# Performance work log

Hardware: AMD Instinct MI355X
Metric: run time of the kernel (lower is better)

Reference implementation:

```python
import jax, jax.numpy as jnp
import numpy as np
import math

B, T, E = 2, 2048, 2048
G, QPG, D = 4, 4, 128  # kv groups, queries per group, head dim (G*QPG*D == E)


def sinusoidal_pe(t, d, dtype):
    pos = jnp.arange(t, dtype=jnp.float32)[:, None]            # [T,1]
    i = jnp.arange(0, d, 2, dtype=jnp.float32)                 # [D/2]
    inv_freq = jnp.exp(-(jnp.log(10000.0) * i / d))            # [D/2]
    ang = pos * inv_freq                                       # [T,D/2]
    pe = jnp.zeros((t, d), dtype=jnp.float32)
    pe = pe.at[:, 0::2].set(jnp.sin(ang)).at[:, 1::2].set(jnp.cos(ang))
    return pe.astype(dtype)


def setup_inputs() -> dict:
    key = jax.random.key(0)
    ks = jax.random.split(key, 6)
    s = lambda fan_in: 1.0 / math.sqrt(fan_in)
    return {
        "x":   jax.random.normal(ks[0], (B, T, E), dtype=jnp.float32),
        "wq":  jax.random.uniform(ks[1], (E, G * QPG * D), jnp.float32, -s(E), s(E)),
        "bq":  jax.random.uniform(ks[2], (G * QPG * D,), jnp.float32, -s(E), s(E)),
        "wkv": jax.random.uniform(ks[3], (E, 2 * G * D), jnp.float32, -s(E), s(E)),
        "bkv": jax.random.uniform(ks[4], (2 * G * D,), jnp.float32, -s(E), s(E)),
        "wo":  jax.random.uniform(ks[5], (G * QPG * D, E), jnp.float32, -s(G * QPG * D), s(G * QPG * D)),
    }


def reference(x, wq, bq, wkv, bkv, wo):
    b, t, e = x.shape
    # projections
    q = (x @ wq + bq).reshape(b, t, G, QPG, D).transpose(0, 2, 3, 1, 4)   # [B,G,QPG,T,D]
    kv = (x @ wkv + bkv).reshape(b, t, G, 1, 2 * D).transpose(0, 2, 3, 1, 4)  # [B,G,1,T,2D]
    k, v = kv[..., :D], kv[..., D:]                                       # [B,G,1,T,D]
    # inline additive sinusoidal positional embedding on q and k
    pe = sinusoidal_pe(t, D, x.dtype)                                     # [T,D]
    q = q + pe
    k = k + pe
    # scores: [B,G,QPG,T,T] (kv head axis k has size 1, summed out)
    scores = jnp.einsum('bgqtd,bgksd->bgqts', q, k) / math.sqrt(D)
    causal = jnp.tril(jnp.ones((t, t), dtype=bool))                       # [T,T]
    scores = jnp.where(causal, scores, -jnp.inf)
    probs = jax.nn.softmax(scores, axis=-1)
    out = jnp.einsum('bgqts,bgksd->btgqd', probs, v).reshape(b, t, G * QPG * D)
    return out @ wo
```

## Files before the change

### kernel.cpp

```cpp
#include <hip/hip_runtime.h>
#include <stdint.h>

typedef __bf16 bf16;
typedef __bf16 bf16x4 __attribute__((ext_vector_type(4)));
typedef __bf16 bf16x8 __attribute__((ext_vector_type(8)));
typedef float floatx4 __attribute__((ext_vector_type(4)));

#define B_   2
#define T_   2048
#define E_   2048
#define G_   4
#define QPG_ 4
#define D_   128
#define H_   16
#define NQ   2048
#define NKV  1024
#define NQKV 3072
#define M_   4096

__device__ __forceinline__ void gload_lds16(const void* g, void* l) {
  __builtin_amdgcn_global_load_lds(
      (__attribute__((address_space(1))) unsigned int*)g,
      (__attribute__((address_space(3))) unsigned int*)l,
      16, 0, 0);
}

__device__ __forceinline__ int swz_stage_col(int lane) {
  return (((lane & 3) ^ ((lane >> 2) & 3) ^ ((lane >> 4) & 3))) * 8;
}


__global__ void cast_f32_bf16(const float* __restrict__ in, bf16* __restrict__ out, int n4) {
  int i = blockIdx.x * blockDim.x + threadIdx.x;
  if (i < n4) {
    float4 v = ((const float4*)in)[i];
    bf16x4 o = {(bf16)v.x, (bf16)v.y, (bf16)v.z, (bf16)v.w};
    ((bf16x4*)out)[i] = o;
  }
}

__global__ void transpose_cast(const float* __restrict__ in, bf16* __restrict__ out,
                               int R, int C, int out_stride) {
  __shared__ float tile[64][65];
  int r0 = blockIdx.x * 64, c0 = blockIdx.y * 64;
  int tx = threadIdx.x & 63, ty = threadIdx.x >> 6;
  for (int i = ty; i < 64; i += 4)
    tile[i][tx] = in[(size_t)(r0 + i) * C + c0 + tx];
  __syncthreads();
  for (int i = ty; i < 64; i += 4)
    out[(size_t)(c0 + i) * out_stride + r0 + tx] = (bf16)tile[tx][i];
}

__global__ void concat_bias(const float* __restrict__ bq, const float* __restrict__ bkv,
                            float* __restrict__ out) {
  int i = blockIdx.x * 256 + threadIdx.x;
  out[i] = (i < NQ) ? bq[i] : bkv[i - NQ];
}


template <int OUT_BF16, int HAS_BIAS>
__global__ __launch_bounds__(256, 2) void gemm_bt(
    const bf16* __restrict__ A, const bf16* __restrict__ Bt,
    const float* __restrict__ bias, void* __restrict__ Cout,
    int M, int N, int K) {
  __shared__ __align__(16) bf16 As[128 * 32];
  __shared__ __align__(16) bf16 Bs[128 * 32];
  const int tid = threadIdx.x;
  const int wave = tid >> 6, lane = tid & 63;
  const int quad = lane >> 4, c = lane & 15;
  const int m0 = blockIdx.x * 128, n0 = blockIdx.y * 128;
  const int wr = (wave >> 1) * 64, wc = (wave & 1) * 64;
  const int xsl = ((quad ^ (c & 3) ^ ((c >> 2) & 3)) & 3) * 8;

  floatx4 acc[4][4];
#pragma unroll
  for (int i = 0; i < 4; ++i)
#pragma unroll
    for (int j = 0; j < 4; ++j) acc[i][j] = (floatx4){0.f, 0.f, 0.f, 0.f};

  const int srow = wave * 32 + (lane >> 2);
  const int scol = swz_stage_col(lane);
  const bf16* Ap = A + (size_t)(m0 + srow) * K + scol;
  const bf16* Bp = Bt + (size_t)(n0 + srow) * K + scol;

  for (int k0 = 0; k0 < K; k0 += 32) {
#pragma unroll
    for (int ch = 0; ch < 2; ++ch) {
      gload_lds16(Ap + (size_t)ch * 16 * K + k0, &As[(wave * 2 + ch) * 512]);
      gload_lds16(Bp + (size_t)ch * 16 * K + k0, &Bs[(wave * 2 + ch) * 512]);
    }
    __syncthreads();
    bf16x8 af[4], bfr[4];
#pragma unroll
    for (int i = 0; i < 4; ++i) {
      af[i]  = *(const bf16x8*)(&As[(wr + i * 16 + c) * 32 + xsl]);
      bfr[i] = *(const bf16x8*)(&Bs[(wc + i * 16 + c) * 32 + xsl]);
    }
#pragma unroll
    for (int mi = 0; mi < 4; ++mi)
#pragma unroll
      for (int ni = 0; ni < 4; ++ni)
        acc[mi][ni] = __builtin_amdgcn_mfma_f32_16x16x32_bf16(af[mi], bfr[ni], acc[mi][ni], 0, 0, 0);
    __syncthreads();
  }

  float bv[4] = {0.f, 0.f, 0.f, 0.f};
  if (HAS_BIAS) {
#pragma unroll
    for (int ni = 0; ni < 4; ++ni) bv[ni] = bias[n0 + wc + ni * 16 + c];
  }
#pragma unroll
  for (int mi = 0; mi < 4; ++mi) {
#pragma unroll
    for (int ni = 0; ni < 4; ++ni) {
      const int col = n0 + wc + ni * 16 + c;
#pragma unroll
      for (int r = 0; r < 4; ++r) {
        const int row = m0 + wr + mi * 16 + quad * 4 + r;
        float v = acc[mi][ni][r] + bv[ni];
        if (OUT_BF16)
          ((bf16*)Cout)[(size_t)row * N + col] = (bf16)v;
        else
          ((float*)Cout)[(size_t)row * N + col] = v;
      }
    }
  }
}


__device__ __forceinline__ float pe_val(int t, int d) {
  int i2 = d & ~1;
  float inv = __expf(-9.210340371976184f * (float)i2 * (1.0f / 128.0f));
  float ang = (float)t * inv;
  return (d & 1) ? cosf(ang) : sinf(ang);
}

__global__ void scatter_qk(const bf16* __restrict__ qkv,
                           bf16* __restrict__ Qb, bf16* __restrict__ Kb) {
  const int row = blockIdx.x;
  const int b = row >> 11, t = row & 2047;
  const int tid = threadIdx.x;
  const int d = tid & 127;
  const float scale = 0.12751745f;
  const float pe = pe_val(t, d);
  for (int h = tid >> 7; h < H_; h += 2) {
    float q = (float)qkv[(size_t)row * NQKV + h * 128 + d] + pe;
    Qb[((size_t)(b * H_ + h) * T_ + t) * D_ + d] = (bf16)(q * scale);
  }
  for (int g = tid >> 7; g < G_; g += 2) {
    float k = (float)qkv[(size_t)row * NQKV + NQ + g * 256 + d] + pe;
    Kb[((size_t)(b * G_ + g) * T_ + t) * D_ + d] = (bf16)k;
  }
}

__global__ void build_vt(const bf16* __restrict__ qkv, bf16* __restrict__ Vt) {
  __shared__ float tile[64][65];
  int t0 = blockIdx.x * 64, d0 = blockIdx.y * 64;
  int bg = blockIdx.z, b = bg >> 2, g = bg & 3;
  const bf16* src = qkv + (size_t)b * T_ * NQKV + NQ + g * 256 + 128;
  bf16* dst = Vt + (size_t)bg * D_ * T_;
  int tx = threadIdx.x & 63, ty = threadIdx.x >> 6;
  for (int i = ty; i < 64; i += 4)
    tile[i][tx] = (float)src[(size_t)(t0 + i) * NQKV + d0 + tx];
  __syncthreads();
  for (int i = ty; i < 64; i += 4)
    dst[(size_t)(d0 + i) * T_ + t0 + tx] = (bf16)tile[tx][i];
}


__global__ __launch_bounds__(512, 4) void flash_attn(
    const bf16* __restrict__ Qb, const bf16* __restrict__ Kb,
    const bf16* __restrict__ Vt, bf16* __restrict__ Ob) {
  const int i = blockIdx.x;
  const int p = i >> 5;
  const int bh = i & 31;
  const int b = bh >> 4, h = bh & 15, g2 = h >> 2;
  const int tid = threadIdx.x;
  const int wave = tid >> 6, lane = tid & 63;
  const int grp = wave >> 2, w4 = wave & 3;
  const int quad = lane >> 4, c = lane & 15;
  const int xsl = ((quad ^ (c & 3) ^ ((c >> 2) & 3)) & 3) * 8;

  __shared__ __align__(16) char smem[75776];
  bf16* Ks = (bf16*)smem;
  bf16* Vs = (bf16*)(smem + 32768);
  bf16* Pq = (bf16*)(smem + 65536);

  const bf16* Kg = Kb + (size_t)(b * G_ + g2) * T_ * D_;
  const bf16* Vg = Vt + (size_t)(b * G_ + g2) * D_ * T_;
  const int slr = lane >> 2;
  const int slc = swz_stage_col(lane);

  auto stage = [&](int tt, int bu) {
    const int k0 = tt * 32;
    bf16* kd = Ks + ((grp * 2 + bu) * 4 + w4) * 1024;
    bf16* vd = Vs + ((grp * 2 + bu) * 4 + w4) * 1024;
#pragma unroll
    for (int hh = 0; hh < 2; ++hh) {
      gload_lds16(Kg + (size_t)(k0 + hh * 16 + slr) * D_ + w4 * 32 + slc, kd + hh * 512);
      gload_lds16(Vg + (size_t)(w4 * 32 + hh * 16 + slr) * T_ + k0 + slc, vd + hh * 512);
    }
  };

  for (int ph = 0; ph < 2; ++ph) {
    const int qt = ph ? (31 - p) : p;
    const int q0 = qt * 64;
    if (ph) __syncthreads();

    const bf16* Qbase = Qb + ((size_t)(b * H_ + h) * T_ + q0 + w4 * 16 + c) * D_;
    bf16x8 qf[4];
#pragma unroll
    for (int ks = 0; ks < 4; ++ks)
      qf[ks] = *(const bf16x8*)(Qbase + ks * 32 + quad * 8);

    floatx4 acc[8];
#pragma unroll
    for (int nd = 0; nd < 8; ++nd) acc[nd] = (floatx4){0.f, 0.f, 0.f, 0.f};
    float rsum[4] = {0.f, 0.f, 0.f, 0.f};

    const int ng = qt + 1;
    const int jbase = grp * ng;
    const int amax = 2 * qt + (w4 >> 1);

    stage(jbase, 0);

    for (int jg = 0; jg < ng; ++jg) {
      __syncthreads();
      if (jg + 1 < ng) stage(jbase + jg + 1, (jg + 1) & 1);
      const int j = jbase + jg;
      if (j > amax) continue;

      const bf16* Kt  = Ks + (grp * 2 + (jg & 1)) * 4096;
      const bf16* Vtl = Vs + (grp * 2 + (jg & 1)) * 4096;

      floatx4 s[2];
      s[0] = (floatx4){0.f, 0.f, 0.f, 0.f};
      s[1] = (floatx4){0.f, 0.f, 0.f, 0.f};
#pragma unroll
      for (int ks = 0; ks < 4; ++ks)
#pragma unroll
        for (int n = 0; n < 2; ++n) {
          bf16x8 kf = *(const bf16x8*)(Kt + ks * 1024 + (n * 16 + c) * 32 + xsl);
          s[n] = __builtin_amdgcn_mfma_f32_16x16x32_bf16(qf[ks], kf, s[n], 0, 0, 0);
        }

      if (j == amax) {
        const int colb = j * 32;
        const int rowb = q0 + w4 * 16 + quad * 4;
#pragma unroll
        for (int n = 0; n < 2; ++n)
#pragma unroll
          for (int r = 0; r < 4; ++r)
            if (colb + n * 16 + c > rowb + r) s[n][r] = -1e30f;
      }

      bf16* Pw = Pq + wave * 640;
#pragma unroll
      for (int n = 0; n < 2; ++n)
#pragma unroll
        for (int r = 0; r < 4; ++r) {
          float pv = exp2f(s[n][r]);
          rsum[r] += pv;
          Pw[(quad * 4 + r) * 40 + n * 16 + c] = (bf16)pv;
        }

      bf16x8 pf = *(const bf16x8*)(&Pw[c * 40 + quad * 8]);

#pragma unroll
      for (int nd = 0; nd < 8; ++nd) {
        bf16x8 vf = *(const bf16x8*)(Vtl + (nd >> 1) * 1024 + ((nd & 1) * 16 + c) * 32 + xsl);
        acc[nd] = __builtin_amdgcn_mfma_f32_16x16x32_bf16(pf, vf, acc[nd], 0, 0, 0);
      }
    }

#pragma unroll
    for (int off = 1; off < 16; off <<= 1)
#pragma unroll
      for (int r = 0; r < 4; ++r) rsum[r] += __shfl_xor(rsum[r], off);

    __syncthreads();
    float* mrg = (float*)smem;
    float* mrs = (float*)(smem + 34816);
    const int row16 = w4 * 16 + quad * 4;

    if (grp == 0) {
#pragma unroll
      for (int nd2 = 0; nd2 < 4; ++nd2)
#pragma unroll
        for (int r = 0; r < 4; ++r)
          mrg[(row16 + r) * 68 + nd2 * 16 + c] = acc[4 + nd2][r];
    } else {
#pragma unroll
      for (int nd2 = 0; nd2 < 4; ++nd2)
#pragma unroll
        for (int r = 0; r < 4; ++r)
          mrg[(64 + row16 + r) * 68 + nd2 * 16 + c] = acc[nd2][r];
    }
    if (c == 0) {
#pragma unroll
      for (int r = 0; r < 4; ++r) mrs[grp * 64 + row16 + r] = rsum[r];
    }
    __syncthreads();

    const int og = grp ^ 1;
    float linv[4];
#pragma unroll
    for (int r = 0; r < 4; ++r) linv[r] = 1.f / (rsum[r] + mrs[og * 64 + row16 + r]);

    if (grp == 0) {
#pragma unroll
      for (int nd2 = 0; nd2 < 4; ++nd2)
#pragma unroll
        for (int r = 0; r < 4; ++r) {
          float o = acc[nd2][r] + mrg[(64 + row16 + r) * 68 + nd2 * 16 + c];
          const int trow = q0 + row16 + r;
          Ob[((size_t)(b * T_ + trow)) * NQ + h * D_ + nd2 * 16 + c] = (bf16)(o * linv[r]);
        }
    } else {
#pragma unroll
      for (int nd2 = 0; nd2 < 4; ++nd2)
#pragma unroll
        for (int r = 0; r < 4; ++r) {
          float o = acc[4 + nd2][r] + mrg[(row16 + r) * 68 + nd2 * 16 + c];
          const int trow = q0 + row16 + r;
          Ob[((size_t)(b * T_ + trow)) * NQ + h * D_ + (4 + nd2) * 16 + c] = (bf16)(o * linv[r]);
        }
    }
  }
}


extern "C" void kernel_launch(void* const* d_in, const int* in_sizes, int n_in,
                              void* d_out, int out_size, void* d_ws, size_t ws_size,
                              hipStream_t stream) {
  const float* x   = (const float*)d_in[0];
  const float* wq  = (const float*)d_in[1];
  const float* bq  = (const float*)d_in[2];
  const float* wkv = (const float*)d_in[3];
  const float* bkv = (const float*)d_in[4];
  const float* wo  = (const float*)d_in[5];
  float* out = (float*)d_out;

  char* p = (char*)d_ws;
  bf16* xb    = (bf16*)p; p += (size_t)M_ * E_ * 2;
  bf16* wqkvT = (bf16*)p; p += (size_t)NQKV * E_ * 2;
  bf16* woT   = (bf16*)p; p += (size_t)E_ * NQ * 2;
  float* biasq = (float*)p; p += 16384;
  bf16* qkv   = (bf16*)p; p += (size_t)M_ * NQKV * 2;
  bf16* Qb    = (bf16*)p; p += (size_t)B_ * H_ * T_ * D_ * 2;
  bf16* Kb    = (bf16*)p; p += (size_t)B_ * G_ * T_ * D_ * 2;
  bf16* Vtb   = (bf16*)p; p += (size_t)B_ * G_ * D_ * T_ * 2;
  bf16* Ob    = (bf16*)p; p += (size_t)M_ * NQ * 2;

  cast_f32_bf16<<<(M_ * E_ / 4) / 256, 256, 0, stream>>>(x, xb, M_ * E_ / 4);
  transpose_cast<<<dim3(E_ / 64, E_ / 64), 256, 0, stream>>>(wq, wqkvT, E_, E_, E_);
  transpose_cast<<<dim3(E_ / 64, NKV / 64), 256, 0, stream>>>(wkv, wqkvT + (size_t)NQ * E_, E_, NKV, E_);
  transpose_cast<<<dim3(E_ / 64, E_ / 64), 256, 0, stream>>>(wo, woT, NQ, E_, NQ);
  concat_bias<<<NQKV / 256, 256, 0, stream>>>(bq, bkv, biasq);

  gemm_bt<1, 1><<<dim3(M_ / 128, NQKV / 128), 256, 0, stream>>>(xb, wqkvT, biasq, qkv, M_, NQKV, E_);
  scatter_qk<<<M_, 256, 0, stream>>>(qkv, Qb, Kb);
  build_vt<<<dim3(T_ / 64, D_ / 64, B_ * G_), 256, 0, stream>>>(qkv, Vtb);
  flash_attn<<<512, 512, 0, stream>>>(Qb, Kb, Vtb, Ob);
  gemm_bt<0, 0><<<dim3(M_ / 128, E_ / 128), 256, 0, stream>>>(Ob, woT, nullptr, out, M_, E_, NQ);
}
```

Before: 312.7 us.

## Load K tiles directly into registers and swizzle P staging in LDS

K tiles are no longer staged through LDS. Each wave loads its K fragments from global memory straight into registers and prefetches the next tile after the QK MFMAs. Only V stays double-buffered in LDS, which shrinks shared memory from about 74KB to 42KB and may allow more blocks per CU. The P scratch layout is also XOR-swizzled to cut LDS bank conflicts. The cost is extra VGPRs for the K fragments and global-load latency exposed inside the loop.

```diff
diff --git a/kernel.cpp b/kernel.cpp
--- a/kernel.cpp
+++ b/kernel.cpp
@@ -181,25 +181,21 @@
   const int quad = lane >> 4, c = lane & 15;
   const int xsl = ((quad ^ (c & 3) ^ ((c >> 2) & 3)) & 3) * 8;
 
-  __shared__ __align__(16) char smem[75776];
-  bf16* Ks = (bf16*)smem;
-  bf16* Vs = (bf16*)(smem + 32768);
-  bf16* Pq = (bf16*)(smem + 65536);
+  __shared__ __align__(16) char smem[43008];
+  bf16* Vs = (bf16*)smem;
+  bf16* Pq = (bf16*)(smem + 32768);
 
   const bf16* Kg = Kb + (size_t)(b * G_ + g2) * T_ * D_;
   const bf16* Vg = Vt + (size_t)(b * G_ + g2) * D_ * T_;
   const int slr = lane >> 2;
   const int slc = swz_stage_col(lane);
 
-  auto stage = [&](int tt, int bu) {
+  auto stageV = [&](int tt, int bu) {
     const int k0 = tt * 32;
-    bf16* kd = Ks + ((grp * 2 + bu) * 4 + w4) * 1024;
     bf16* vd = Vs + ((grp * 2 + bu) * 4 + w4) * 1024;
 #pragma unroll
-    for (int hh = 0; hh < 2; ++hh) {
-      gload_lds16(Kg + (size_t)(k0 + hh * 16 + slr) * D_ + w4 * 32 + slc, kd + hh * 512);
+    for (int hh = 0; hh < 2; ++hh)
       gload_lds16(Vg + (size_t)(w4 * 32 + hh * 16 + slr) * T_ + k0 + slc, vd + hh * 512);
-    }
   };
 
   for (int ph = 0; ph < 2; ++ph) {
@@ -222,15 +218,22 @@
     const int jbase = grp * ng;
     const int amax = 2 * qt + (w4 >> 1);
 
-    stage(jbase, 0);
+    bf16x8 kreg[8];
+#pragma unroll
+    for (int ks = 0; ks < 4; ++ks)
+#pragma unroll
+      for (int n = 0; n < 2; ++n)
+        kreg[ks * 2 + n] = *(const bf16x8*)(
+            Kg + (size_t)(jbase * 32 + n * 16 + c) * D_ + ks * 32 + quad * 8);
+
+    stageV(jbase, 0);
 
     for (int jg = 0; jg < ng; ++jg) {
       __syncthreads();
-      if (jg + 1 < ng) stage(jbase + jg + 1, (jg + 1) & 1);
+      if (jg + 1 < ng) stageV(jbase + jg + 1, (jg + 1) & 1);
       const int j = jbase + jg;
       if (j > amax) continue;
 
-      const bf16* Kt  = Ks + (grp * 2 + (jg & 1)) * 4096;
       const bf16* Vtl = Vs + (grp * 2 + (jg & 1)) * 4096;
 
       floatx4 s[2];
@@ -239,10 +242,19 @@
 #pragma unroll
       for (int ks = 0; ks < 4; ++ks)
 #pragma unroll
-        for (int n = 0; n < 2; ++n) {
-          bf16x8 kf = *(const bf16x8*)(Kt + ks * 1024 + (n * 16 + c) * 32 + xsl);
-          s[n] = __builtin_amdgcn_mfma_f32_16x16x32_bf16(qf[ks], kf, s[n], 0, 0, 0);
-        }
+        for (int n = 0; n < 2; ++n)
+          s[n] = __builtin_amdgcn_mfma_f32_16x16x32_bf16(qf[ks], kreg[ks * 2 + n], s[n], 0, 0, 0);
+
+      __builtin_amdgcn_sched_barrier(0);
+      if (jg + 1 < ng && j + 1 <= amax) {
+        const int k0n = (j + 1) * 32;
+#pragma unroll
+        for (int ks = 0; ks < 4; ++ks)
+#pragma unroll
+          for (int n = 0; n < 2; ++n)
+            kreg[ks * 2 + n] = *(const bf16x8*)(
+                Kg + (size_t)(k0n + n * 16 + c) * D_ + ks * 32 + quad * 8);
+      }
 
       if (j == amax) {
         const int colb = j * 32;
@@ -261,10 +273,11 @@
         for (int r = 0; r < 4; ++r) {
           float pv = exp2f(s[n][r]);
           rsum[r] += pv;
-          Pw[(quad * 4 + r) * 40 + n * 16 + c] = (bf16)pv;
+          const int chs = (n * 2 + (c >> 3)) ^ quad;
+          Pw[(quad * 4 + r) * 40 + chs * 8 + (c & 7)] = (bf16)pv;
         }
 
-      bf16x8 pf = *(const bf16x8*)(&Pw[c * 40 + quad * 8]);
+      bf16x8 pf = *(const bf16x8*)(&Pw[c * 40 + (quad ^ (c >> 2)) * 8]);
 
 #pragma unroll
       for (int nd = 0; nd < 8; ++nd) {
```

Measured after the change: 391.1 us. 25.0% more time.
